# Performance work log

Measured on AMD Instinct MI355X. Metric: run time of the kernel, lower is better.

## Reference

```python
import jax, jax.numpy as jnp
import numpy as np

NB, FD, NR, L = 4, 128, 4, 4
CUT, CUT3, NE = 5.0, 4.0, 108
N_ATOMS, N_EDGES, N_ANGLES, N_GRAPHS = 8000, 200000, 400000, 100
BONDS_PER, ANGLES_PER = 2000, 4000

def swish(x):
    return x * jax.nn.sigmoid(x)

def cutoff_fn(r, rc):
    x = r / rc
    return 1.0 - 6.0 * x**5 + 15.0 * x**4 - 10.0 * x**3

def rbf(r):
    # smooth Bessel basis, [E, NR+1]
    n = jnp.arange(1, NR + 2, dtype=r.dtype)
    return jnp.sqrt(2.0 / CUT) * jnp.sin(n * jnp.pi * r[:, None] / CUT) / r[:, None]

def shrb(r, cos_t):
    # spherical-harmonic (Legendre, l=0..3) x radial Bessel (n=1..4) -> [A, 16]
    n = jnp.arange(1, NR + 1, dtype=r.dtype)
    rad = jnp.sin(n * jnp.pi * r[:, None] / CUT3) / r[:, None]
    ang = jnp.stack([jnp.ones_like(cos_t), cos_t, 0.5 * (3.0 * cos_t**2 - 1.0), 0.5 * (5.0 * cos_t**3 - 3.0 * cos_t)], axis=1)
    feat = (rad[:, :, None] * ang[:, None, :]).reshape(r.shape[0], NR * L)
    return feat * cutoff_fn(r, CUT3)[:, None]

def setup_inputs() -> dict:
    key = jax.random.key(0)
    ks = jax.random.split(key, 24)
    def nrm(k, shape, fan):
        return jax.random.normal(k, shape, jnp.float32) / np.sqrt(fan).astype(np.float32)
    return {
        'atomic_numbers': jax.random.randint(ks[0], (N_ATOMS,), 0, NE, jnp.int32),
        'edge_index': jax.random.randint(ks[1], (2, N_EDGES), 0, N_ATOMS, jnp.int32),
        'edge_dist': jax.random.uniform(ks[2], (N_EDGES,), jnp.float32, 0.5, CUT),
        'three_body_indices': jax.random.randint(ks[3], (N_ANGLES, 2), 0, BONDS_PER, jnp.int32),
        'norm_ik': jax.random.uniform(ks[4], (N_ANGLES,), jnp.float32, 0.5, CUT3),
        'cos_angles': jax.random.uniform(ks[5], (N_ANGLES,), jnp.float32, -1.0, 1.0),
        'total_num_bonds': jnp.full((N_GRAPHS,), BONDS_PER, jnp.int32),
        'total_num_angles': jnp.full((N_GRAPHS,), ANGLES_PER, jnp.int32),
        'emb': nrm(ks[6], (NE, FD), 1.0),
        'W_enc': nrm(ks[7], (NR + 1, FD), NR + 1), 'b_enc': jnp.zeros((FD,), jnp.float32),
        'W_angle': nrm(ks[8], (NB, NR * L, FD), NR * L),
        'Wg': nrm(ks[9], (NB, FD, FD), FD), 'bg': jnp.zeros((NB, FD), jnp.float32),
        'W_tb': nrm(ks[10], (NB, FD, FD), FD), 'b_tb': jnp.zeros((NB, FD), jnp.float32),
        'We1': nrm(ks[11], (NB, 3 * FD, FD), 3 * FD), 'be1': jnp.zeros((NB, FD), jnp.float32),
        'We0': nrm(ks[12], (NB, NR + 1, FD), NR + 1),
        'Wa1': nrm(ks[13], (NB, 3 * FD, FD), 3 * FD), 'ba1': jnp.zeros((NB, FD), jnp.float32),
        'Wa0': nrm(ks[14], (NB, NR + 1, FD), NR + 1),
        'W1': nrm(ks[15], (FD, FD), FD), 'b1': jnp.zeros((FD,), jnp.float32),
        'W2': nrm(ks[16], (FD, FD), FD), 'b2': jnp.zeros((FD,), jnp.float32),
        'W3': nrm(ks[17], (FD, 1), FD), 'b3': jnp.zeros((1,), jnp.float32),
    }

def reference(atomic_numbers, edge_index, edge_dist, three_body_indices, norm_ik, cos_angles, total_num_bonds, total_num_angles, emb, W_enc, b_enc, W_angle, Wg, bg, W_tb, b_tb, We1, be1, We0, Wa1, ba1, Wa0, W1, b1, W2, b2, W3, b3):
    E, N, A = edge_dist.shape[0], atomic_numbers.shape[0], norm_ik.shape[0]
    # ragged three-body index offsets (cumsum over per-graph bond counts)
    cum = jnp.cumsum(total_num_bonds)
    off = jnp.concatenate([jnp.zeros((1,), cum.dtype), cum[:-1]])
    off_a = jnp.repeat(off, total_num_angles, total_repeat_length=A)
    tbi = three_body_indices + off_a[:, None].astype(three_body_indices.dtype)
    idx_ij, idx_ik = tbi[:, 0], tbi[:, 1]
    send, recv = edge_index[0], edge_index[1]
    ef0 = rbf(edge_dist)                      # [E, 5]
    e = swish(ef0 @ W_enc + b_enc)            # [E, FD]
    v = emb[atomic_numbers]                   # [N, FD]
    ang = shrb(norm_ik, cos_angles)           # [A, 16]
    fc_ik = cutoff_fn(norm_ik, CUT3)          # [A]
    for b in range(NB):
        # three-body interaction: angle -> center bond ij
        k_atom = recv[idx_ik]
        gate = jax.nn.sigmoid(v[k_atom] @ Wg[b] + bg[b])            # [A, FD]
        msg = (ang @ W_angle[b]) * gate * fc_ik[:, None]            # [A, FD]
        agg = jax.ops.segment_sum(msg, idx_ij, num_segments=E)      # [E, FD]
        e = e + swish(agg @ W_tb[b] + b_tb[b])
        # gated graph conv: edge update then atom update
        vi, vj = v[send], v[recv]
        h = jnp.concatenate([vi, vj, e], axis=1)                    # [E, 3FD]
        e = e + swish(h @ We1[b] + be1[b]) * (ef0 @ We0[b])
        h2 = jnp.concatenate([vi, vj, e], axis=1)
        m = swish(h2 @ Wa1[b] + ba1[b]) * (ef0 @ Wa0[b])
        v = v + jax.ops.segment_sum(m, recv, num_segments=N)
    # per-atom energy readout
    h = swish(v @ W1 + b1)
    h = swish(h @ W2 + b2)
    return h @ W3 + b3                                              # [N, 1]
```

## Files before the change

### kernel.cpp

```cpp
#include <hip/hip_runtime.h>


typedef short short8 __attribute__((ext_vector_type(8)));
typedef float f32x4v __attribute__((ext_vector_type(4)));

__device__ __forceinline__ float sigmoidf_(float x) { return 1.0f / (1.0f + __expf(-x)); }
__device__ __forceinline__ float swishf_(float x) { return x * sigmoidf_(x); }

__device__ __forceinline__ unsigned short f2bf(float x) {
    unsigned int u = __float_as_uint(x);
    unsigned int r = (u + 0x7FFFu + ((u >> 16) & 1u)) >> 16;
    return (unsigned short)r;
}
__device__ __forceinline__ float bf2f(unsigned short u) {
    return __uint_as_float(((unsigned int)u) << 16);
}
__device__ __forceinline__ float blo(unsigned int u) { return __uint_as_float(u << 16); }
__device__ __forceinline__ float bhi(unsigned int u) { return __uint_as_float(u & 0xffff0000u); }
__device__ __forceinline__ unsigned int pk2(float a, float b) {
    return (unsigned int)f2bf(a) | ((unsigned int)f2bf(b) << 16);
}
__device__ __forceinline__ unsigned int addbf2(unsigned int a, unsigned int b) {
    return pk2(blo(a) + blo(b), bhi(a) + bhi(b));
}

__device__ __forceinline__ f32x4v mfma_bf16(short8 a, short8 b, f32x4v c) {
    return __builtin_amdgcn_mfma_f32_16x16x32_bf16(a, b, c, 0, 0, 0);
}

__device__ __forceinline__ float4 f4add(float4 a, float4 b) {
    return make_float4(a.x + b.x, a.y + b.y, a.z + b.z, a.w + b.w);
}
__device__ __forceinline__ float4 f4swish(float4 a) {
    return make_float4(swishf_(a.x), swishf_(a.y), swishf_(a.z), swishf_(a.w));
}
__device__ __forceinline__ float getc(const float4& v, int i) {
    return i == 0 ? v.x : (i == 1 ? v.y : (i == 2 ? v.z : v.w));
}

#define FMA4(J, A) \
    acc[J].x = fmaf(A, bv.x, acc[J].x); acc[J].y = fmaf(A, bv.y, acc[J].y); \
    acc[J].z = fmaf(A, bv.z, acc[J].z); acc[J].w = fmaf(A, bv.w, acc[J].w)

template <int S>
__device__ __forceinline__ void gemm32f(const float* As, const float* __restrict__ B,
                                        int tm, int f0, float4 acc[4]) {
#pragma unroll 4
    for (int k = 0; k < 128; ++k) {
        const float4 a0 = *(const float4*)(As + k * S + (tm << 2));
        const float4 bv = *(const float4*)(B + (k << 7) + f0);
        FMA4(0, a0.x); FMA4(1, a0.y); FMA4(2, a0.z); FMA4(3, a0.w);
    }
}

#define ANG_PROJ(AP, M0, M1)                                                     \
    {                                                                            \
        const float4 A0 = (AP)[0], A1 = (AP)[1], A2 = (AP)[2], A3 = (AP)[3];     \
        float m0, m1;                                                            \
        m0 = A0.x * wc[0].x;  m1 = A0.x * wc[0].y;                               \
        m0 = fmaf(A0.y, wc[1].x, m0);  m1 = fmaf(A0.y, wc[1].y, m1);             \
        m0 = fmaf(A0.z, wc[2].x, m0);  m1 = fmaf(A0.z, wc[2].y, m1);             \
        m0 = fmaf(A0.w, wc[3].x, m0);  m1 = fmaf(A0.w, wc[3].y, m1);             \
        m0 = fmaf(A1.x, wc[4].x, m0);  m1 = fmaf(A1.x, wc[4].y, m1);             \
        m0 = fmaf(A1.y, wc[5].x, m0);  m1 = fmaf(A1.y, wc[5].y, m1);             \
        m0 = fmaf(A1.z, wc[6].x, m0);  m1 = fmaf(A1.z, wc[6].y, m1);             \
        m0 = fmaf(A1.w, wc[7].x, m0);  m1 = fmaf(A1.w, wc[7].y, m1);             \
        m0 = fmaf(A2.x, wc[8].x, m0);  m1 = fmaf(A2.x, wc[8].y, m1);             \
        m0 = fmaf(A2.y, wc[9].x, m0);  m1 = fmaf(A2.y, wc[9].y, m1);             \
        m0 = fmaf(A2.z, wc[10].x, m0); m1 = fmaf(A2.z, wc[10].y, m1);            \
        m0 = fmaf(A2.w, wc[11].x, m0); m1 = fmaf(A2.w, wc[11].y, m1);            \
        m0 = fmaf(A3.x, wc[12].x, m0); m1 = fmaf(A3.x, wc[12].y, m1);            \
        m0 = fmaf(A3.y, wc[13].x, m0); m1 = fmaf(A3.y, wc[13].y, m1);            \
        m0 = fmaf(A3.z, wc[14].x, m0); m1 = fmaf(A3.z, wc[14].y, m1);            \
        m0 = fmaf(A3.w, wc[15].x, m0); m1 = fmaf(A3.w, wc[15].y, m1);            \
        (M0) = m0; (M1) = m1;                                                    \
    }

__global__ void k_offsets(const int* __restrict__ tnb, const int* __restrict__ tna,
                          int NG, int* __restrict__ boff, int* __restrict__ acum) {
    if (threadIdx.x == 0 && blockIdx.x == 0) {
        int ab = 0, aa = 0;
        for (int g = 0; g < NG; ++g) {
            boff[g] = ab;
            ab += tnb[g];
            aa += tna[g];
            acum[g] = aa;
        }
    }
}

__global__ void k_angle_setup(const int* __restrict__ tb, const float* __restrict__ rnorm,
                              const float* __restrict__ cosang, const int* __restrict__ ei,
                              int E, int A, int NG,
                              const int* __restrict__ boff, const int* __restrict__ acum,
                              float* __restrict__ ang,
                              int* __restrict__ kat, int* __restrict__ iij,
                              int* __restrict__ cnt) {
    const int a = blockIdx.x * 256 + threadIdx.x;
    if (a >= A) return;
    int lo = 0, hi = NG - 1;
    while (lo < hi) {
        const int mid = (lo + hi) >> 1;
        if (a < acum[mid]) hi = mid; else lo = mid + 1;
    }
    const int off = boff[lo];
    iij[a] = tb[2 * a] + off;
    kat[a] = ei[(size_t)E + tb[2 * a + 1] + off];
    atomicAdd(&cnt[tb[2 * a] + off], 1);

    const float r = rnorm[a], c = cosang[a];
    const float rinv = 1.0f / r;
    const float x = r * 0.25f;
    const float fc = 1.0f + x * x * x * (-10.0f + x * (15.0f - 6.0f * x));
    const float fc2 = fc * fc;
    const float p2 = 1.5f * c * c - 0.5f;
    const float p3 = 2.5f * c * c * c - 1.5f * c;
    float4* ap = (float4*)(ang + (size_t)a * 16);
#pragma unroll
    for (int n = 0; n < 4; ++n) {
        const float rad = __sinf(r * (float)(n + 1) * 0.7853981633974483f) * rinv * fc2;
        ap[n] = make_float4(rad, rad * c, rad * p2, rad * p3);
    }
}

__global__ void k_scan1(const int* __restrict__ cnt, int* __restrict__ start,
                        int* __restrict__ bsum, int n) {
    __shared__ int sh[256];
    const int t = threadIdx.x;
    const int base = blockIdx.x * 2048 + t * 8;
    int v[8], s = 0;
#pragma unroll
    for (int i = 0; i < 8; ++i) { v[i] = (base + i < n) ? cnt[base + i] : 0; s += v[i]; }
    sh[t] = s;
    __syncthreads();
    for (int off = 1; off < 256; off <<= 1) {
        int x = (t >= off) ? sh[t - off] : 0;
        __syncthreads();
        sh[t] += x;
        __syncthreads();
    }
    if (t == 255) bsum[blockIdx.x] = sh[255];
    int run = sh[t] - s;
#pragma unroll
    for (int i = 0; i < 8; ++i) { if (base + i < n) start[base + i] = run; run += v[i]; }
}

__global__ void k_scan2(int* __restrict__ bsum, int nb) {
    __shared__ int sh[256];
    const int t = threadIdx.x;
    int v = (t < nb) ? bsum[t] : 0;
    sh[t] = v;
    __syncthreads();
    for (int off = 1; off < 256; off <<= 1) {
        int x = (t >= off) ? sh[t - off] : 0;
        __syncthreads();
        sh[t] += x;
        __syncthreads();
    }
    if (t < nb) bsum[t] = sh[t] - v;
}

__global__ void k_scan3(int* __restrict__ start, const int* __restrict__ bsum, int n) {
    const int i = blockIdx.x * 256 + threadIdx.x;
    if (i < n) start[i] += bsum[i >> 11];
}

__global__ void k_scatter(const float* __restrict__ ang,
                          const int* __restrict__ kat, const int* __restrict__ iij,
                          const int* __restrict__ start, int* __restrict__ fill,
                          float* __restrict__ angS, int* __restrict__ katS, int A) {
    const int a = blockIdx.x * 256 + threadIdx.x;
    if (a >= A) return;
    const int ij = iij[a];
    const int pos = start[ij] + atomicAdd(&fill[ij], 1);
    const float4* src = (const float4*)(ang + (size_t)a * 16);
    float4* dst = (float4*)(angS + (size_t)pos * 16);
#pragma unroll
    for (int j = 0; j < 4; ++j) dst[j] = src[j];
    katS[pos] = kat[a];
}

__global__ void k_hist_recv(const int* __restrict__ ei, int E, int* __restrict__ cntR) {
    const int e = blockIdx.x * 256 + threadIdx.x;
    if (e < E) atomicAdd(&cntR[ei[(size_t)E + e]], 1);
}

__global__ void k_scatter_recv(const int* __restrict__ ei, int E,
                               const int* __restrict__ startR, int* __restrict__ fillR,
                               int* __restrict__ epos) {
    const int e = blockIdx.x * 256 + threadIdx.x;
    if (e < E) {
        const int r = ei[(size_t)E + e];
        epos[e] = startR[r] + atomicAdd(&fillR[r], 1);
    }
}

__global__ void k_pack(const float* __restrict__ Wg, const float* __restrict__ Wtb,
                       const float* __restrict__ We1, const float* __restrict__ Wa1,
                       unsigned short* __restrict__ Bpk) {
    const int gid = blockIdx.x * 256 + threadIdx.x;
    const int mat = gid >> 11;
    const int t2 = gid & 2047;
    const int b = mat >> 3, which = mat & 7;
    const float* W;
    switch (which) {
        case 0: W = Wg + (size_t)b * 16384; break;
        case 1: W = We1 + (size_t)b * 49152; break;
        case 2: W = We1 + (size_t)b * 49152 + 16384; break;
        case 3: W = Wa1 + (size_t)b * 49152; break;
        case 4: W = Wa1 + (size_t)b * 49152 + 16384; break;
        case 5: W = Wtb + (size_t)b * 16384; break;
        case 6: W = We1 + (size_t)b * 49152 + 32768; break;
        default: W = Wa1 + (size_t)b * 49152 + 32768; break;
    }
    const int kc = t2 >> 9, nt = (t2 >> 6) & 7, lane = t2 & 63;
    const int q = lane >> 4, cc = lane & 15;
    const int col = nt * 16 + cc;
    union { unsigned short us[8]; uint4 v; } pk;
#pragma unroll
    for (int j = 0; j < 8; ++j)
        pk.us[j] = f2bf(W[(size_t)(kc * 32 + q * 8 + j) * 128 + col]);
    *(uint4*)(Bpk + (size_t)mat * 16384 + (size_t)((kc * 8 + nt) * 64 + lane) * 8) = pk.v;
}

__global__ void k_edge_init(const float* __restrict__ dist, const float* __restrict__ Wenc,
                            const float* __restrict__ benc, unsigned int* __restrict__ ePq,
                            float* __restrict__ ef0) {
    __shared__ float sarr[16][5];
    const int s = blockIdx.x, t = threadIdx.x;
    if (t < 16) {
        const float r = dist[s * 16 + t];
        const float rinv = 1.0f / r;
#pragma unroll
        for (int n = 0; n < 5; ++n) {
            const float v = 0.6324555320336759f * __sinf(r * (float)(n + 1) * 0.6283185307179586f) * rinv;
            sarr[t][n] = v;
            ef0[(size_t)(s * 16 + t) * 5 + n] = v;
        }
    }
    __syncthreads();
    const int lane = t >> 3, nt = t & 7;
    const int q = lane >> 4;
    const int f = nt * 16 + (lane & 15);
    float wv[5];
#pragma unroll
    for (int n = 0; n < 5; ++n) wv[n] = Wenc[n * 128 + f];
    const float bz = benc[f];
    float o[4];
#pragma unroll
    for (int r = 0; r < 4; ++r) {
        const int m = q * 4 + r;
        float acc = bz;
#pragma unroll
        for (int n = 0; n < 5; ++n) acc = fmaf(sarr[m][n], wv[n], acc);
        o[r] = swishf_(acc);
    }
    unsigned int* epB = ePq + (size_t)s * 1024;
    epB[(nt * 2) * 64 + lane] = pk2(o[0], o[1]);
    epB[(nt * 2 + 1) * 64 + lane] = pk2(o[2], o[3]);
}

__global__ void k_atom_init(const int* __restrict__ an, const float* __restrict__ emb,
                            float* __restrict__ v, unsigned int* __restrict__ vq, int N) {
    const size_t gid = (size_t)blockIdx.x * 256 + threadIdx.x;
    if (gid >= (size_t)N * 64) return;
    const int a = (int)(gid >> 6), j = (int)(gid & 63);
    const float2 e = *(const float2*)(emb + (size_t)an[a] * 128 + 2 * j);
    *(float2*)(v + (size_t)a * 128 + 2 * j) = e;
    vq[gid] = pk2(e.x, e.y);
}

__global__ void __launch_bounds__(256, 4) k_atom_pre(
    const unsigned int* __restrict__ vq,
    const unsigned short* __restrict__ Bpk5, const float* __restrict__ bg,
    unsigned int* __restrict__ Gq, unsigned int* __restrict__ Pe1q,
    unsigned int* __restrict__ Pe2q,
    unsigned int* __restrict__ Pa1q, unsigned int* __restrict__ Pa2q) {
    __shared__ __align__(16) unsigned short At[64 * 136];
    unsigned int* At32 = (unsigned int*)At;
    const int t = threadIdx.x;
    const int w = t >> 6, l = t & 63;
    const int q = l >> 4, c = l & 15;
    const int g = blockIdx.y;
    const int abase = blockIdx.x * 64 + 16 * w;

    const unsigned short* vh = (const unsigned short*)vq;
    short8 af[4];
#pragma unroll
    for (int kc = 0; kc < 4; ++kc)
        af[kc] = *(const short8*)(vh + (size_t)(abase + c) * 128 + kc * 32 + q * 8);

    const short8* Bp = (const short8*)(Bpk5 + (size_t)g * 16384);
    const f32x4v zz = {0.0f, 0.0f, 0.0f, 0.0f};
    f32x4v acc[8];
#pragma unroll
    for (int nt = 0; nt < 8; ++nt) acc[nt] = zz;
#pragma unroll
    for (int nt = 0; nt < 8; ++nt)
#pragma unroll
        for (int kc = 0; kc < 4; ++kc)
            acc[nt] = mfma_bf16(af[kc], Bp[(kc * 8 + nt) * 64 + l], acc[nt]);

    unsigned int* OUT = (g == 0) ? Gq : (g == 1) ? Pe1q : (g == 2) ? Pe2q
                      : (g == 3) ? Pa1q : Pa2q;
#pragma unroll
    for (int nt = 0; nt < 8; ++nt) {
        const int fo = nt * 16 + c;
        if (g == 0) {
            const float bz = bg[fo];
#pragma unroll
            for (int r = 0; r < 4; ++r)
                At[(16 * w + q * 4 + r) * 136 + fo] = f2bf(sigmoidf_(acc[nt][r] + bz));
        } else {
#pragma unroll
            for (int r = 0; r < 4; ++r)
                At[(16 * w + q * 4 + r) * 136 + fo] = f2bf(acc[nt][r]);
        }
    }
#pragma unroll
    for (int j = 0; j < 16; ++j)
        OUT[(size_t)(abase + j) * 64 + l] = At32[(16 * w + j) * 68 + l];
}

__global__ void __launch_bounds__(256, 4) k_edge(
    const float* __restrict__ angS, const int* __restrict__ katS,
    const int* __restrict__ startA, const int* __restrict__ cntA,
    const unsigned int* __restrict__ Gq, const float* __restrict__ Wang,
    const float* __restrict__ ef0g,
    unsigned int* __restrict__ ePq, const int* __restrict__ ei, int E,
    const unsigned int* __restrict__ Pe1q, const unsigned int* __restrict__ Pe2q,
    const unsigned int* __restrict__ Pa1q, const unsigned int* __restrict__ Pa2q,
    const int* __restrict__ epos,
    const unsigned short* __restrict__ Bpk3,
    const float* __restrict__ btb, const float* __restrict__ be1,
    const float* __restrict__ We0, const float* __restrict__ ba1,
    const float* __restrict__ Wa0, unsigned int* __restrict__ mPq) {
    __shared__ __align__(16) unsigned short At[64 * 136];
    __shared__ __align__(16) unsigned short sPh[64 * 136];
    __shared__ float sef0[320];
    __shared__ int sA0[64], sAn[64];
    unsigned int* At32 = (unsigned int*)At;
    unsigned int* sP32 = (unsigned int*)sPh;

    const int t = threadIdx.x;
    const int w = t >> 6, l = t & 63;
    const int q = l >> 4, c = l & 15;
    const int g4 = l >> 4, l16 = l & 15;
    const size_t base = (size_t)blockIdx.x * 64;
    const int wbase = (int)base + 16 * w;

    for (int i = t; i < 320; i += 256) sef0[i] = ef0g[base * 5 + i];
    if (l < 16) {
        sA0[16 * w + l] = startA[wbase + l];
        sAn[16 * w + l] = cntA[wbase + l];
    }

#define STAGE_SP(P1, P2)                                                         \
    _Pragma("unroll") for (int i = 0; i < 4; ++i) {                              \
        const int j = i * 4 + g4;                                                \
        const int es_ = ei[wbase + j];                                           \
        const int rc_ = ei[(size_t)E + wbase + j];                               \
        const uint4 u1 = *(const uint4*)((P1) + (size_t)es_ * 64 + l16 * 4);     \
        const uint4 u2 = *(const uint4*)((P2) + (size_t)rc_ * 64 + l16 * 4);     \
        uint4 o;                                                                 \
        o.x = addbf2(u1.x, u2.x); o.y = addbf2(u1.y, u2.y);                      \
        o.z = addbf2(u1.z, u2.z); o.w = addbf2(u1.w, u2.w);                      \
        *(uint4*)(sP32 + (16 * w + j) * 68 + l16 * 4) = o;                       \
    }

    STAGE_SP(Pe1q, Pe2q)
    unsigned int* epB = ePq + (size_t)(blockIdx.x * 4 + w) * 1024;

    {
        float2 wc[16];
#pragma unroll
        for (int k = 0; k < 16; ++k) wc[k] = *(const float2*)(Wang + k * 128 + 2 * l);

        int j = 0;
        const int aBeg = __builtin_amdgcn_readfirstlane(sA0[16 * w]);
        const int aEnd = __builtin_amdgcn_readfirstlane(sA0[16 * w + 15] + sAn[16 * w + 15]);
        int nextB = __builtin_amdgcn_readfirstlane(sA0[16 * w] + sAn[16 * w]);
        float aa0 = 0.0f, aa1 = 0.0f;

#define FLUSH_TO(AIDX)                                                           \
        while ((AIDX) >= nextB && j < 15) {                                      \
            At32[(16 * w + j) * 68 + l] = pk2(aa0, aa1);                         \
            aa0 = 0.0f; aa1 = 0.0f;                                              \
            ++j;                                                                 \
            nextB = __builtin_amdgcn_readfirstlane(sA0[16 * w + j] + sAn[16 * w + j]); \
        }

        int a = aBeg;
        for (; a + 1 < aEnd; a += 2) {
            const int ka0 = __builtin_amdgcn_readfirstlane(katS[a]);
            const int ka1 = __builtin_amdgcn_readfirstlane(katS[a + 1]);
            const unsigned int gv0 = Gq[(size_t)ka0 * 64 + l];
            const unsigned int gv1 = Gq[(size_t)ka1 * 64 + l];
            const float4* ap0 = (const float4*)(angS + (size_t)a * 16);
            const float4* ap1 = (const float4*)(angS + (size_t)(a + 1) * 16);
            float m0a, m1a, m0b, m1b;
            ANG_PROJ(ap0, m0a, m1a)
            ANG_PROJ(ap1, m0b, m1b)
            FLUSH_TO(a)
            aa0 = fmaf(m0a, blo(gv0), aa0);
            aa1 = fmaf(m1a, bhi(gv0), aa1);
            FLUSH_TO(a + 1)
            aa0 = fmaf(m0b, blo(gv1), aa0);
            aa1 = fmaf(m1b, bhi(gv1), aa1);
        }
        if (a < aEnd) {
            const int ka0 = __builtin_amdgcn_readfirstlane(katS[a]);
            const unsigned int gv0 = Gq[(size_t)ka0 * 64 + l];
            const float4* ap0 = (const float4*)(angS + (size_t)a * 16);
            float m0a, m1a;
            ANG_PROJ(ap0, m0a, m1a)
            FLUSH_TO(a)
            aa0 = fmaf(m0a, blo(gv0), aa0);
            aa1 = fmaf(m1a, bhi(gv0), aa1);
        }
        At32[(16 * w + j) * 68 + l] = pk2(aa0, aa1);
        for (int jj = j + 1; jj < 16; ++jj) At32[(16 * w + jj) * 68 + l] = 0u;
#undef FLUSH_TO
    }
    __syncthreads();

    const short8* Bp1 = (const short8*)Bpk3;
    const short8* Bp2 = Bp1 + 2048;
    const short8* Bp3 = Bp2 + 2048;
    const f32x4v zz = {0.0f, 0.0f, 0.0f, 0.0f};

    short8 af[4];
#define LOAD_AF                                                                  \
    _Pragma("unroll") for (int kc = 0; kc < 4; ++kc)                             \
        af[kc] = *(const short8*)(At + (16 * w + c) * 136 + kc * 32 + q * 8);
#define TRANSPOSE_ER2                                                            \
    _Pragma("unroll") for (int nt = 0; nt < 8; ++nt) {                           \
        At[(16 * w + q * 4 + 0) * 136 + nt * 16 + c] = (unsigned short)er2[2 * nt];        \
        At[(16 * w + q * 4 + 1) * 136 + nt * 16 + c] = (unsigned short)(er2[2 * nt] >> 16);\
        At[(16 * w + q * 4 + 2) * 136 + nt * 16 + c] = (unsigned short)er2[2 * nt + 1];    \
        At[(16 * w + q * 4 + 3) * 136 + nt * 16 + c] = (unsigned short)(er2[2 * nt + 1] >> 16);\
    }

    unsigned int er2[16];

    LOAD_AF
#pragma unroll 1
    for (int h = 0; h < 2; ++h) {
        f32x4v acc[4];
#pragma unroll
        for (int n2 = 0; n2 < 4; ++n2) acc[n2] = zz;
#pragma unroll
        for (int n2 = 0; n2 < 4; ++n2)
#pragma unroll
            for (int kc = 0; kc < 4; ++kc)
                acc[n2] = mfma_bf16(af[kc], Bp1[(kc * 8 + h * 4 + n2) * 64 + l], acc[n2]);
#pragma unroll
        for (int n2 = 0; n2 < 4; ++n2) {
            const int nt = h * 4 + n2;
            const unsigned int e0 = epB[(2 * nt) * 64 + l];
            const unsigned int e1 = epB[(2 * nt + 1) * 64 + l];
            const float bt = btb[nt * 16 + c];
            er2[2 * nt] = pk2(blo(e0) + swishf_(acc[n2][0] + bt),
                              bhi(e0) + swishf_(acc[n2][1] + bt));
            er2[2 * nt + 1] = pk2(blo(e1) + swishf_(acc[n2][2] + bt),
                                  bhi(e1) + swishf_(acc[n2][3] + bt));
        }
    }
    TRANSPOSE_ER2

    float efs[4][5];
#pragma unroll
    for (int r = 0; r < 4; ++r)
#pragma unroll
        for (int n = 0; n < 5; ++n) efs[r][n] = sef0[(16 * w + q * 4 + r) * 5 + n];

    LOAD_AF
#pragma unroll 1
    for (int h = 0; h < 2; ++h) {
        f32x4v acc[4];
#pragma unroll
        for (int n2 = 0; n2 < 4; ++n2) acc[n2] = zz;
#pragma unroll
        for (int n2 = 0; n2 < 4; ++n2)
#pragma unroll
            for (int kc = 0; kc < 4; ++kc)
                acc[n2] = mfma_bf16(af[kc], Bp2[(kc * 8 + h * 4 + n2) * 64 + l], acc[n2]);
#pragma unroll
        for (int n2 = 0; n2 < 4; ++n2) {
            const int nt = h * 4 + n2;
            const int fo = nt * 16 + c;
            const float bt = be1[fo];
            const float w0 = We0[fo], w1 = We0[128 + fo], w2 = We0[256 + fo],
                        w3 = We0[384 + fo], w4 = We0[512 + fo];
            float vv[4];
#pragma unroll
            for (int r = 0; r < 4; ++r) {
                const float p12 = bf2f(sPh[(16 * w + q * 4 + r) * 136 + fo]);
                const float x = acc[n2][r] + bt + p12;
                float sc = efs[r][0] * w0;
                sc = fmaf(efs[r][1], w1, sc);
                sc = fmaf(efs[r][2], w2, sc);
                sc = fmaf(efs[r][3], w3, sc);
                sc = fmaf(efs[r][4], w4, sc);
                const unsigned int eold = er2[2 * nt + (r >> 1)];
                const float eb = (r & 1) ? bhi(eold) : blo(eold);
                vv[r] = eb + swishf_(x) * sc;
            }
            er2[2 * nt] = pk2(vv[0], vv[1]);
            er2[2 * nt + 1] = pk2(vv[2], vv[3]);
            epB[(2 * nt) * 64 + l] = er2[2 * nt];
            epB[(2 * nt + 1) * 64 + l] = er2[2 * nt + 1];
        }
    }
    STAGE_SP(Pa1q, Pa2q)
    TRANSPOSE_ER2

    LOAD_AF
#pragma unroll 1
    for (int h = 0; h < 2; ++h) {
        f32x4v acc[4];
#pragma unroll
        for (int n2 = 0; n2 < 4; ++n2) acc[n2] = zz;
#pragma unroll
        for (int n2 = 0; n2 < 4; ++n2)
#pragma unroll
            for (int kc = 0; kc < 4; ++kc)
                acc[n2] = mfma_bf16(af[kc], Bp3[(kc * 8 + h * 4 + n2) * 64 + l], acc[n2]);
#pragma unroll
        for (int n2 = 0; n2 < 4; ++n2) {
            const int nt = h * 4 + n2;
            const int fo = nt * 16 + c;
            const float bt = ba1[fo];
            const float w0 = Wa0[fo], w1 = Wa0[128 + fo], w2 = Wa0[256 + fo],
                        w3 = Wa0[384 + fo], w4 = Wa0[512 + fo];
#pragma unroll
            for (int r = 0; r < 4; ++r) {
                const float p12 = bf2f(sPh[(16 * w + q * 4 + r) * 136 + fo]);
                const float x = acc[n2][r] + bt + p12;
                float sc = efs[r][0] * w0;
                sc = fmaf(efs[r][1], w1, sc);
                sc = fmaf(efs[r][2], w2, sc);
                sc = fmaf(efs[r][3], w3, sc);
                sc = fmaf(efs[r][4], w4, sc);
                At[(16 * w + q * 4 + r) * 136 + fo] = f2bf(swishf_(x) * sc);
            }
        }
    }
#pragma unroll
    for (int j = 0; j < 16; ++j) {
        const int ep = epos[wbase + j];
        mPq[(size_t)ep * 64 + l] = At32[(16 * w + j) * 68 + l];
    }
#undef LOAD_AF
#undef TRANSPOSE_ER2
#undef STAGE_SP
}

__global__ void k_dvagg(const unsigned int* __restrict__ mPq,
                        const int* __restrict__ startR, const int* __restrict__ cntR,
                        float* __restrict__ v, unsigned int* __restrict__ vq, int N) {
    const int a = blockIdx.x * 4 + (threadIdx.x >> 6);
    if (a >= N) return;
    const int l = threadIdx.x & 63;
    const int s0 = startR[a], n = cntR[a];
    float a0 = 0.0f, a1 = 0.0f;
    for (int i = 0; i < n; ++i) {
        const unsigned int u = mPq[(size_t)(s0 + i) * 64 + l];
        a0 += blo(u);
        a1 += bhi(u);
    }
    const float v0 = v[(size_t)a * 128 + 2 * l] + a0;
    const float v1 = v[(size_t)a * 128 + 2 * l + 1] + a1;
    v[(size_t)a * 128 + 2 * l] = v0;
    v[(size_t)a * 128 + 2 * l + 1] = v1;
    vq[(size_t)a * 64 + l] = pk2(v0, v1);
}

__global__ void k_readout(const float* __restrict__ v,
                          const float* __restrict__ W1, const float* __restrict__ b1,
                          const float* __restrict__ W2, const float* __restrict__ b2,
                          const float* __restrict__ W3, const float* __restrict__ b3,
                          float* __restrict__ out) {
    __shared__ float At[128 * 36];
    const int t = threadIdx.x;
    const int tn = t & 31, tm = t >> 5;
    const int f0 = tn << 2;
    const size_t base = (size_t)blockIdx.x * 32;
    {
        const int m = t & 31, cb = t >> 5;
        const float4* src = (const float4*)(v + (base + m) * 128);
#pragma unroll
        for (int i = 0; i < 4; ++i) {
            const int c = cb + (i << 3);
            const float4 ld = src[c];
            float* dst = At + (c << 2) * 32 + m;
            dst[0] = ld.x; dst[32] = ld.y; dst[64] = ld.z; dst[96] = ld.w;
        }
    }
    __syncthreads();
    float4 acc[4] = {};
    gemm32f<32>(At, W1, tm, f0, acc);
    {
        const float4 bv1 = *(const float4*)(b1 + f0);
#pragma unroll
        for (int j = 0; j < 4; ++j) acc[j] = f4swish(f4add(acc[j], bv1));
    }
    __syncthreads();
#pragma unroll
    for (int i = 0; i < 4; ++i) {
        float4 w0;
        w0.x = getc(acc[0], i); w0.y = getc(acc[1], i); w0.z = getc(acc[2], i); w0.w = getc(acc[3], i);
        *(float4*)(At + (f0 + i) * 36 + (tm << 2)) = w0;
    }
    __syncthreads();
    float4 acc2[4] = {};
    gemm32f<36>(At, W2, tm, f0, acc2);
    const float4 bv2 = *(const float4*)(b2 + f0);
    const float4 w3v = *(const float4*)(W3 + f0);
#pragma unroll
    for (int j = 0; j < 4; ++j) {
        const float4 h = f4swish(f4add(acc2[j], bv2));
        float p = h.x * w3v.x + h.y * w3v.y + h.z * w3v.z + h.w * w3v.w;
        p += __shfl_xor(p, 16);
        p += __shfl_xor(p, 8);
        p += __shfl_xor(p, 4);
        p += __shfl_xor(p, 2);
        p += __shfl_xor(p, 1);
        if (tn == 0) out[base + (tm << 2) + j] = p + b3[0];
    }
}

extern "C" void kernel_launch(void* const* d_in, const int* in_sizes, int n_in,
                              void* d_out, int out_size, void* d_ws, size_t ws_size,
                              hipStream_t stream) {
    const int N = in_sizes[0];
    const int E = in_sizes[2];
    const int A = in_sizes[4];
    const int NG = in_sizes[6];

    const int* an = (const int*)d_in[0];
    const int* ei = (const int*)d_in[1];
    const float* dist = (const float*)d_in[2];
    const int* tb = (const int*)d_in[3];
    const float* rnorm = (const float*)d_in[4];
    const float* cosang = (const float*)d_in[5];
    const int* tnb = (const int*)d_in[6];
    const int* tna = (const int*)d_in[7];
    const float* emb = (const float*)d_in[8];
    const float* Wenc = (const float*)d_in[9];
    const float* benc = (const float*)d_in[10];
    const float* Wang = (const float*)d_in[11];
    const float* Wg = (const float*)d_in[12];
    const float* bg = (const float*)d_in[13];
    const float* Wtb = (const float*)d_in[14];
    const float* btb = (const float*)d_in[15];
    const float* We1 = (const float*)d_in[16];
    const float* be1 = (const float*)d_in[17];
    const float* We0 = (const float*)d_in[18];
    const float* Wa1 = (const float*)d_in[19];
    const float* ba1 = (const float*)d_in[20];
    const float* Wa0 = (const float*)d_in[21];
    const float* W1 = (const float*)d_in[22];
    const float* b1 = (const float*)d_in[23];
    const float* W2 = (const float*)d_in[24];
    const float* b2 = (const float*)d_in[25];
    const float* W3 = (const float*)d_in[26];
    const float* b3 = (const float*)d_in[27];
    float* out = (float*)d_out;

    float* ws = (float*)d_ws;
    size_t off = 0;
    auto alloc = [&](size_t n) { float* p = ws + off; off += (n + 3) & ~(size_t)3; return p; };
    unsigned int* ePq = (unsigned int*)alloc((size_t)E * 64);
    unsigned int* mPq = (unsigned int*)alloc((size_t)E * 64);
    float* v_ = alloc((size_t)N * 128);
    unsigned int* vq = (unsigned int*)alloc((size_t)N * 64);
    unsigned int* Gq = (unsigned int*)alloc((size_t)N * 64);
    unsigned int* Pe1q = (unsigned int*)alloc((size_t)N * 64);
    unsigned int* Pe2q = (unsigned int*)alloc((size_t)N * 64);
    unsigned int* Pa1q = (unsigned int*)alloc((size_t)N * 64);
    unsigned int* Pa2q = (unsigned int*)alloc((size_t)N * 64);
    float* ef0 = alloc((size_t)E * 5);
    float* ang = alloc((size_t)A * 16);
    float* angS = alloc((size_t)A * 16);
    int* kat = (int*)alloc((size_t)A);
    int* katS = (int*)alloc((size_t)A);
    int* iij = (int*)alloc((size_t)A);
    int* cnt = (int*)alloc((size_t)E);
    int* start = (int*)alloc((size_t)E);
    int* fill = (int*)alloc((size_t)E);
    int* cntR = (int*)alloc((size_t)N);
    int* startR = (int*)alloc((size_t)N);
    int* fillR = (int*)alloc((size_t)N);
    int* epos = (int*)alloc((size_t)E);
    int* bsum = (int*)alloc(512);
    int* boff = (int*)alloc(256);
    int* acum = boff + 128;
    unsigned short* Bpk = (unsigned short*)alloc((size_t)32 * 8192);

    const int nscanE = (E + 2047) / 2048;
    const int nscanR = (N + 2047) / 2048;

    (void)hipMemsetAsync(cnt, 0, (size_t)E * 4, stream);
    (void)hipMemsetAsync(fill, 0, (size_t)E * 4, stream);
    (void)hipMemsetAsync(cntR, 0, (size_t)N * 4, stream);
    (void)hipMemsetAsync(fillR, 0, (size_t)N * 4, stream);
    k_offsets<<<1, 64, 0, stream>>>(tnb, tna, NG, boff, acum);
    k_angle_setup<<<(A + 255) / 256, 256, 0, stream>>>(tb, rnorm, cosang, ei, E, A, NG,
                                                       boff, acum, ang, kat, iij, cnt);
    k_scan1<<<nscanE, 256, 0, stream>>>(cnt, start, bsum, E);
    k_scan2<<<1, 256, 0, stream>>>(bsum, nscanE);
    k_scan3<<<(E + 255) / 256, 256, 0, stream>>>(start, bsum, E);
    k_scatter<<<(A + 255) / 256, 256, 0, stream>>>(ang, kat, iij, start, fill, angS, katS, A);
    k_hist_recv<<<(E + 255) / 256, 256, 0, stream>>>(ei, E, cntR);
    k_scan1<<<nscanR, 256, 0, stream>>>(cntR, startR, bsum, N);
    k_scan2<<<1, 256, 0, stream>>>(bsum, nscanR);
    k_scan3<<<(N + 255) / 256, 256, 0, stream>>>(startR, bsum, N);
    k_scatter_recv<<<(E + 255) / 256, 256, 0, stream>>>(ei, E, startR, fillR, epos);
    k_pack<<<256, 256, 0, stream>>>(Wg, Wtb, We1, Wa1, Bpk);
    k_edge_init<<<E / 16, 512, 0, stream>>>(dist, Wenc, benc, ePq, ef0);
    k_atom_init<<<(int)(((size_t)N * 64 + 255) / 256), 256, 0, stream>>>(an, emb, v_, vq, N);

    for (int b = 0; b < 4; ++b) {
        k_atom_pre<<<dim3(N / 64, 5), 256, 0, stream>>>(
            vq, Bpk + (size_t)(b * 8) * 16384, bg + b * 128,
            Gq, Pe1q, Pe2q, Pa1q, Pa2q);
        k_edge<<<E / 64, 256, 0, stream>>>(
            angS, katS, start, cnt, Gq, Wang + (size_t)b * 2048, ef0,
            ePq, ei, E, Pe1q, Pe2q, Pa1q, Pa2q, epos,
            Bpk + (size_t)(b * 8 + 5) * 16384,
            btb + b * 128, be1 + b * 128, We0 + (size_t)b * 640,
            ba1 + b * 128, Wa0 + (size_t)b * 640, mPq);
        k_dvagg<<<(N + 3) / 4, 256, 0, stream>>>(mPq, startR, cntR, v_, vq, N);
    }
    k_readout<<<N / 32, 256, 0, stream>>>(v_, W1, b1, W2, b2, W3, b3, out);
}
```

Measured before the change: 1.106 ms.

## Compute angle projection with bf16 MFMA and store angle features in bf16

Angle basis features are now stored as bf16, which halves their footprint in the setup, scatter and edge kernels. W_angle is prepacked into MFMA B-fragment layout. The per-lane scalar 16-term dot product in k_edge is replaced with MFMA tiles over 16 angles at a time, staged through LDS before gating and accumulation. This cuts VALU work and angle-feature bandwidth. In exchange it adds bf16 rounding of both the features and the projected messages, an LDS round trip with waits, and the Pe staging is moved after the angle loop so the same shared buffer can be reused.

```diff
diff --git a/kernel.cpp b/kernel.cpp
--- a/kernel.cpp
+++ b/kernel.cpp
@@ -52,29 +52,6 @@
         FMA4(0, a0.x); FMA4(1, a0.y); FMA4(2, a0.z); FMA4(3, a0.w);
     }
 }
-
-#define ANG_PROJ(AP, M0, M1)                                                     \
-    {                                                                            \
-        const float4 A0 = (AP)[0], A1 = (AP)[1], A2 = (AP)[2], A3 = (AP)[3];     \
-        float m0, m1;                                                            \
-        m0 = A0.x * wc[0].x;  m1 = A0.x * wc[0].y;                               \
-        m0 = fmaf(A0.y, wc[1].x, m0);  m1 = fmaf(A0.y, wc[1].y, m1);             \
-        m0 = fmaf(A0.z, wc[2].x, m0);  m1 = fmaf(A0.z, wc[2].y, m1);             \
-        m0 = fmaf(A0.w, wc[3].x, m0);  m1 = fmaf(A0.w, wc[3].y, m1);             \
-        m0 = fmaf(A1.x, wc[4].x, m0);  m1 = fmaf(A1.x, wc[4].y, m1);             \
-        m0 = fmaf(A1.y, wc[5].x, m0);  m1 = fmaf(A1.y, wc[5].y, m1);             \
-        m0 = fmaf(A1.z, wc[6].x, m0);  m1 = fmaf(A1.z, wc[6].y, m1);             \
-        m0 = fmaf(A1.w, wc[7].x, m0);  m1 = fmaf(A1.w, wc[7].y, m1);             \
-        m0 = fmaf(A2.x, wc[8].x, m0);  m1 = fmaf(A2.x, wc[8].y, m1);             \
-        m0 = fmaf(A2.y, wc[9].x, m0);  m1 = fmaf(A2.y, wc[9].y, m1);             \
-        m0 = fmaf(A2.z, wc[10].x, m0); m1 = fmaf(A2.z, wc[10].y, m1);            \
-        m0 = fmaf(A2.w, wc[11].x, m0); m1 = fmaf(A2.w, wc[11].y, m1);            \
-        m0 = fmaf(A3.x, wc[12].x, m0); m1 = fmaf(A3.x, wc[12].y, m1);            \
-        m0 = fmaf(A3.y, wc[13].x, m0); m1 = fmaf(A3.y, wc[13].y, m1);            \
-        m0 = fmaf(A3.z, wc[14].x, m0); m1 = fmaf(A3.z, wc[14].y, m1);            \
-        m0 = fmaf(A3.w, wc[15].x, m0); m1 = fmaf(A3.w, wc[15].y, m1);            \
-        (M0) = m0; (M1) = m1;                                                    \
-    }
 
 __global__ void k_offsets(const int* __restrict__ tnb, const int* __restrict__ tna,
                           int NG, int* __restrict__ boff, int* __restrict__ acum) {
@@ -93,7 +70,7 @@
                               const float* __restrict__ cosang, const int* __restrict__ ei,
                               int E, int A, int NG,
                               const int* __restrict__ boff, const int* __restrict__ acum,
-                              float* __restrict__ ang,
+                              unsigned short* __restrict__ ang,
                               int* __restrict__ kat, int* __restrict__ iij,
                               int* __restrict__ cnt) {
     const int a = blockIdx.x * 256 + threadIdx.x;
@@ -115,12 +92,18 @@
     const float fc2 = fc * fc;
     const float p2 = 1.5f * c * c - 0.5f;
     const float p3 = 2.5f * c * c * c - 1.5f * c;
-    float4* ap = (float4*)(ang + (size_t)a * 16);
+    union { unsigned short us[16]; uint4 v[2]; } pkk;
 #pragma unroll
     for (int n = 0; n < 4; ++n) {
         const float rad = __sinf(r * (float)(n + 1) * 0.7853981633974483f) * rinv * fc2;
-        ap[n] = make_float4(rad, rad * c, rad * p2, rad * p3);
-    }
+        pkk.us[n * 4 + 0] = f2bf(rad);
+        pkk.us[n * 4 + 1] = f2bf(rad * c);
+        pkk.us[n * 4 + 2] = f2bf(rad * p2);
+        pkk.us[n * 4 + 3] = f2bf(rad * p3);
+    }
+    uint4* ap = (uint4*)(ang + (size_t)a * 16);
+    ap[0] = pkk.v[0];
+    ap[1] = pkk.v[1];
 }
 
 __global__ void k_scan1(const int* __restrict__ cnt, int* __restrict__ start,
@@ -165,18 +148,18 @@
     if (i < n) start[i] += bsum[i >> 11];
 }
 
-__global__ void k_scatter(const float* __restrict__ ang,
+__global__ void k_scatter(const unsigned short* __restrict__ ang,
                           const int* __restrict__ kat, const int* __restrict__ iij,
                           const int* __restrict__ start, int* __restrict__ fill,
-                          float* __restrict__ angS, int* __restrict__ katS, int A) {
+                          unsigned short* __restrict__ angS, int* __restrict__ katS, int A) {
     const int a = blockIdx.x * 256 + threadIdx.x;
     if (a >= A) return;
     const int ij = iij[a];
     const int pos = start[ij] + atomicAdd(&fill[ij], 1);
-    const float4* src = (const float4*)(ang + (size_t)a * 16);
-    float4* dst = (float4*)(angS + (size_t)pos * 16);
-#pragma unroll
-    for (int j = 0; j < 4; ++j) dst[j] = src[j];
+    const uint4* src = (const uint4*)(ang + (size_t)a * 16);
+    uint4* dst = (uint4*)(angS + (size_t)pos * 16);
+    dst[0] = src[0];
+    dst[1] = src[1];
     katS[pos] = kat[a];
 }
 
@@ -223,6 +206,20 @@
     *(uint4*)(Bpk + (size_t)mat * 16384 + (size_t)((kc * 8 + nt) * 64 + lane) * 8) = pk.v;
 }
 
+__global__ void k_pack_ang(const float* __restrict__ Wang, unsigned short* __restrict__ Wpk) {
+    const int gid = blockIdx.x * 64 + threadIdx.x;
+    const int b = gid >> 9, nt = (gid >> 6) & 7, lane = gid & 63;
+    const int q = lane >> 4, cc = lane & 15;
+    const int col = nt * 16 + cc;
+    union { unsigned short us[8]; uint4 v; } pk;
+#pragma unroll
+    for (int j = 0; j < 8; ++j) {
+        const int k = q * 8 + j;
+        pk.us[j] = (k < 16) ? f2bf(Wang[(size_t)b * 2048 + k * 128 + col]) : (unsigned short)0;
+    }
+    *(uint4*)(Wpk + (size_t)b * 4096 + (size_t)(nt * 64 + lane) * 8) = pk.v;
+}
+
 __global__ void k_edge_init(const float* __restrict__ dist, const float* __restrict__ Wenc,
                             const float* __restrict__ benc, unsigned int* __restrict__ ePq,
                             float* __restrict__ ef0) {
@@ -323,9 +320,9 @@
 }
 
 __global__ void __launch_bounds__(256, 4) k_edge(
-    const float* __restrict__ angS, const int* __restrict__ katS,
+    const unsigned short* __restrict__ angBS, const int* __restrict__ katS,
     const int* __restrict__ startA, const int* __restrict__ cntA,
-    const unsigned int* __restrict__ Gq, const float* __restrict__ Wang,
+    const unsigned int* __restrict__ Gq, const unsigned short* __restrict__ Wangpk,
     const float* __restrict__ ef0g,
     unsigned int* __restrict__ ePq, const int* __restrict__ ei, int E,
     const unsigned int* __restrict__ Pe1q, const unsigned int* __restrict__ Pe2q,
@@ -348,6 +345,7 @@
     const int g4 = l >> 4, l16 = l & 15;
     const size_t base = (size_t)blockIdx.x * 64;
     const int wbase = (int)base + 16 * w;
+    const f32x4v zz = {0.0f, 0.0f, 0.0f, 0.0f};
 
     for (int i = t; i < 320; i += 256) sef0[i] = ef0g[base * 5 + i];
     if (l < 16) {
@@ -368,19 +366,17 @@
         *(uint4*)(sP32 + (16 * w + j) * 68 + l16 * 4) = o;                       \
     }
 
-    STAGE_SP(Pe1q, Pe2q)
     unsigned int* epB = ePq + (size_t)(blockIdx.x * 4 + w) * 1024;
 
     {
-        float2 wc[16];
-#pragma unroll
-        for (int k = 0; k < 16; ++k) wc[k] = *(const float2*)(Wang + k * 128 + 2 * l);
-
         int j = 0;
         const int aBeg = __builtin_amdgcn_readfirstlane(sA0[16 * w]);
         const int aEnd = __builtin_amdgcn_readfirstlane(sA0[16 * w + 15] + sAn[16 * w + 15]);
         int nextB = __builtin_amdgcn_readfirstlane(sA0[16 * w] + sAn[16 * w]);
         float aa0 = 0.0f, aa1 = 0.0f;
+        const short8* WB = (const short8*)Wangpk;
+        unsigned short* msg = sPh + (16 * w) * 136;
+        unsigned int* msg32 = sP32 + (16 * w) * 68;
 
 #define FLUSH_TO(AIDX)                                                           \
         while ((AIDX) >= nextB && j < 15) {                                      \
@@ -390,44 +386,49 @@
             nextB = __builtin_amdgcn_readfirstlane(sA0[16 * w + j] + sAn[16 * w + j]); \
         }
 
-        int a = aBeg;
-        for (; a + 1 < aEnd; a += 2) {
-            const int ka0 = __builtin_amdgcn_readfirstlane(katS[a]);
-            const int ka1 = __builtin_amdgcn_readfirstlane(katS[a + 1]);
-            const unsigned int gv0 = Gq[(size_t)ka0 * 64 + l];
-            const unsigned int gv1 = Gq[(size_t)ka1 * 64 + l];
-            const float4* ap0 = (const float4*)(angS + (size_t)a * 16);
-            const float4* ap1 = (const float4*)(angS + (size_t)(a + 1) * 16);
-            float m0a, m1a, m0b, m1b;
-            ANG_PROJ(ap0, m0a, m1a)
-            ANG_PROJ(ap1, m0b, m1b)
-            FLUSH_TO(a)
-            aa0 = fmaf(m0a, blo(gv0), aa0);
-            aa1 = fmaf(m1a, bhi(gv0), aa1);
-            FLUSH_TO(a + 1)
-            aa0 = fmaf(m0b, blo(gv1), aa0);
-            aa1 = fmaf(m1b, bhi(gv1), aa1);
-        }
-        if (a < aEnd) {
-            const int ka0 = __builtin_amdgcn_readfirstlane(katS[a]);
-            const unsigned int gv0 = Gq[(size_t)ka0 * 64 + l];
-            const float4* ap0 = (const float4*)(angS + (size_t)a * 16);
-            float m0a, m1a;
-            ANG_PROJ(ap0, m0a, m1a)
-            FLUSH_TO(a)
-            aa0 = fmaf(m0a, blo(gv0), aa0);
-            aa1 = fmaf(m1a, bhi(gv0), aa1);
+        for (int a0 = aBeg; a0 < aEnd; a0 += 16) {
+            short8 afA = {0, 0, 0, 0, 0, 0, 0, 0};
+            if (q < 2 && a0 + c < aEnd)
+                afA = *(const short8*)(angBS + (size_t)(a0 + c) * 16 + q * 8);
+            const int aK = (a0 + c < aEnd) ? a0 + c : aEnd - 1;
+            const int katv = katS[aK];
+
+#pragma unroll
+            for (int nt = 0; nt < 8; ++nt) {
+                f32x4v d = mfma_bf16(afA, WB[nt * 64 + l], zz);
+#pragma unroll
+                for (int r = 0; r < 4; ++r)
+                    msg[(q * 4 + r) * 136 + nt * 16 + c] = f2bf(d[r]);
+            }
+            asm volatile("s_waitcnt lgkmcnt(0)" ::: "memory");
+            __builtin_amdgcn_sched_barrier(0);
+
+            unsigned int mvv[16];
+#pragma unroll
+            for (int r16 = 0; r16 < 16; ++r16) mvv[r16] = msg32[r16 * 68 + l];
+            asm volatile("s_waitcnt lgkmcnt(0)" ::: "memory");
+            __builtin_amdgcn_sched_barrier(0);
+
+#pragma unroll
+            for (int r16 = 0; r16 < 16; ++r16) {
+                const int a = a0 + r16;
+                const int ka = __shfl(katv, r16);
+                const unsigned int gv = Gq[(size_t)ka * 64 + l];
+                FLUSH_TO(a)
+                aa0 = fmaf(blo(mvv[r16]), blo(gv), aa0);
+                aa1 = fmaf(bhi(mvv[r16]), bhi(gv), aa1);
+            }
         }
         At32[(16 * w + j) * 68 + l] = pk2(aa0, aa1);
         for (int jj = j + 1; jj < 16; ++jj) At32[(16 * w + jj) * 68 + l] = 0u;
 #undef FLUSH_TO
     }
+    STAGE_SP(Pe1q, Pe2q)
     __syncthreads();
 
     const short8* Bp1 = (const short8*)Bpk3;
     const short8* Bp2 = Bp1 + 2048;
     const short8* Bp3 = Bp2 + 2048;
-    const f32x4v zz = {0.0f, 0.0f, 0.0f, 0.0f};
 
     short8 af[4];
 #define LOAD_AF                                                                  \
@@ -681,8 +682,8 @@
     unsigned int* Pa1q = (unsigned int*)alloc((size_t)N * 64);
     unsigned int* Pa2q = (unsigned int*)alloc((size_t)N * 64);
     float* ef0 = alloc((size_t)E * 5);
-    float* ang = alloc((size_t)A * 16);
-    float* angS = alloc((size_t)A * 16);
+    unsigned short* angB = (unsigned short*)alloc((size_t)A * 8);
+    unsigned short* angBS = (unsigned short*)alloc((size_t)A * 8);
     int* kat = (int*)alloc((size_t)A);
     int* katS = (int*)alloc((size_t)A);
     int* iij = (int*)alloc((size_t)A);
@@ -697,6 +698,7 @@
     int* boff = (int*)alloc(256);
     int* acum = boff + 128;
     unsigned short* Bpk = (unsigned short*)alloc((size_t)32 * 8192);
+    unsigned short* Wangpk = (unsigned short*)alloc(8192);
 
     const int nscanE = (E + 2047) / 2048;
     const int nscanR = (N + 2047) / 2048;
@@ -707,17 +709,18 @@
     (void)hipMemsetAsync(fillR, 0, (size_t)N * 4, stream);
     k_offsets<<<1, 64, 0, stream>>>(tnb, tna, NG, boff, acum);
     k_angle_setup<<<(A + 255) / 256, 256, 0, stream>>>(tb, rnorm, cosang, ei, E, A, NG,
-                                                       boff, acum, ang, kat, iij, cnt);
+                                                       boff, acum, angB, kat, iij, cnt);
     k_scan1<<<nscanE, 256, 0, stream>>>(cnt, start, bsum, E);
     k_scan2<<<1, 256, 0, stream>>>(bsum, nscanE);
     k_scan3<<<(E + 255) / 256, 256, 0, stream>>>(start, bsum, E);
-    k_scatter<<<(A + 255) / 256, 256, 0, stream>>>(ang, kat, iij, start, fill, angS, katS, A);
+    k_scatter<<<(A + 255) / 256, 256, 0, stream>>>(angB, kat, iij, start, fill, angBS, katS, A);
     k_hist_recv<<<(E + 255) / 256, 256, 0, stream>>>(ei, E, cntR);
     k_scan1<<<nscanR, 256, 0, stream>>>(cntR, startR, bsum, N);
     k_scan2<<<1, 256, 0, stream>>>(bsum, nscanR);
     k_scan3<<<(N + 255) / 256, 256, 0, stream>>>(startR, bsum, N);
     k_scatter_recv<<<(E + 255) / 256, 256, 0, stream>>>(ei, E, startR, fillR, epos);
     k_pack<<<256, 256, 0, stream>>>(Wg, Wtb, We1, Wa1, Bpk);
+    k_pack_ang<<<32, 64, 0, stream>>>(Wang, Wangpk);
     k_edge_init<<<E / 16, 512, 0, stream>>>(dist, Wenc, benc, ePq, ef0);
     k_atom_init<<<(int)(((size_t)N * 64 + 255) / 256), 256, 0, stream>>>(an, emb, v_, vq, N);
 
@@ -726,7 +729,7 @@
             vq, Bpk + (size_t)(b * 8) * 16384, bg + b * 128,
             Gq, Pe1q, Pe2q, Pa1q, Pa2q);
         k_edge<<<E / 64, 256, 0, stream>>>(
-            angS, katS, start, cnt, Gq, Wang + (size_t)b * 2048, ef0,
+            angBS, katS, start, cnt, Gq, Wangpk + (size_t)b * 4096, ef0,
             ePq, ei, E, Pe1q, Pe2q, Pa1q, Pa2q, epos,
             Bpk + (size_t)(b * 8 + 5) * 16384,
             btb + b * 128, be1 + b * 128, We0 + (size_t)b * 640,
```

Measured after the change: 1.029 ms. 1.07x faster.
